# Kernel tuning notes

Hardware: AMD Instinct MI355X
Metric: run time of the kernel (lower is better)

The kernel has to match this reference:

```python
import jax, jax.numpy as jnp
import numpy as np

NUM_HEADS = 16
HEAD_SIZE = 64
N_EMBD = 1024


def setup_inputs() -> dict:
    key = jax.random.key(0)
    ks = jax.random.split(key, 7)
    B, T, S, C, H, D = 4, 1024, 1024, N_EMBD, NUM_HEADS, HEAD_SIZE
    s = 1.0 / np.sqrt(C)
    return {
        "x": jax.random.normal(ks[0], (B, T, C), jnp.float32),
        "y_enc": jax.random.normal(ks[1], (B, S, C), jnp.float32),
        # stacked per-head projection weights [H, C, D]
        "Wq": jax.random.normal(ks[2], (H, C, D), jnp.float32) * s,
        "Wk": jax.random.normal(ks[3], (H, C, D), jnp.float32) * s,
        "Wv": jax.random.normal(ks[4], (H, C, D), jnp.float32) * s,
        "Wo": jax.random.normal(ks[5], (C, C), jnp.float32) * s,
        "bo": jax.random.normal(ks[6], (C,), jnp.float32) * 0.01,
    }


def reference(x, y_enc, Wq, Wk, Wv, Wo, bo):
    B, T, C = x.shape
    # per-head projections (batched over heads)
    q = jnp.einsum("btc,hcd->bhtd", x, Wq)       # [B,H,T,D]
    k = jnp.einsum("bsc,hcd->bhsd", y_enc, Wk)   # [B,H,S,D]
    v = jnp.einsum("bsc,hcd->bhsd", y_enc, Wv)   # [B,H,S,D]
    # NOTE: original scales by C**-0.5 with C = n_embd (full embed dim)
    scale = C ** (-0.5)
    wei = jnp.einsum("bhtd,bhsd->bhts", q, k) * scale
    wei = jax.nn.softmax(wei, axis=-1)
    out = jnp.einsum("bhts,bhsd->bhtd", wei, v)  # [B,H,T,D]
    # concat heads along last dim == transpose + reshape
    out = out.transpose(0, 2, 1, 3).reshape(B, T, -1)  # [B,T,H*D]
    return out @ Wo.T + bo
```

## Files before the change

kernel.cpp:

```cpp
#include <hip/hip_runtime.h>
#include <hip/hip_bf16.h>

using u16 = unsigned short;
typedef short bf16x8 __attribute__((ext_vector_type(8)));
typedef float f32x4 __attribute__((ext_vector_type(4)));
typedef u16 u16x8 __attribute__((ext_vector_type(8)));
typedef u16 u16x4 __attribute__((ext_vector_type(4)));

#define B_ 4
#define T_ 1024
#define S_ 1024
#define C_ 1024
#define H_ 16
#define D_ 64
#define SCALE_LOG2E 0.0450842200f

#define AKSTR 40
#define KSTR  72

__device__ __forceinline__ u16 f2bf(float f) {
    __hip_bfloat16 h = __float2bfloat16(f);
    u16 u; __builtin_memcpy(&u, &h, 2); return u;
}
__device__ __forceinline__ float bf2f(u16 u) {
    __hip_bfloat16 h; __builtin_memcpy(&h, &u, 2);
    return __bfloat162float(h);
}
__device__ __forceinline__ u16x8 ldg8(const u16* p) { return *reinterpret_cast<const u16x8*>(p); }
__device__ __forceinline__ void sts8(u16* p, u16x8 v) { *reinterpret_cast<u16x8*>(p) = v; }
__device__ __forceinline__ bf16x8 lds8(const u16* p) { return *reinterpret_cast<const bf16x8*>(p); }

__global__ __launch_bounds__(256) void prep_kernel(const float* __restrict__ x,
                                                   const float* __restrict__ yenc,
                                                   const float* __restrict__ Wq,
                                                   const float* __restrict__ Wk,
                                                   const float* __restrict__ Wv,
                                                   const float* __restrict__ Wo,
                                                   u16* __restrict__ xbf,
                                                   u16* __restrict__ ybf,
                                                   u16* __restrict__ wtq,
                                                   u16* __restrict__ wtk,
                                                   u16* __restrict__ wtv,
                                                   u16* __restrict__ wohi,
                                                   u16* __restrict__ wolo) {
    const int z = blockIdx.z;
    const int t = threadIdx.x;
    if (z < 3) {
        __shared__ float ldsT[64][65];
        const float* W = (z == 0) ? Wq : (z == 1) ? Wk : Wv;
        u16* Wt = (z == 0) ? wtq : (z == 1) ? wtk : wtv;
        const int c0 = blockIdx.x * 64;
        const int h  = blockIdx.y;
        const float* Wh = W + (size_t)h * C_ * D_;
        u16* Wth = Wt + (size_t)h * D_ * C_;
        {
            int c = t >> 2;
            int d0 = (t & 3) * 16;
            #pragma unroll
            for (int q = 0; q < 4; ++q) {
                float4 v = *reinterpret_cast<const float4*>(Wh + (size_t)(c0 + c) * D_ + d0 + q * 4);
                ldsT[d0 + q * 4 + 0][c] = v.x;
                ldsT[d0 + q * 4 + 1][c] = v.y;
                ldsT[d0 + q * 4 + 2][c] = v.z;
                ldsT[d0 + q * 4 + 3][c] = v.w;
            }
        }
        __syncthreads();
        {
            int d = t >> 2;
            int cq = (t & 3) * 16;
            u16x8 o0, o1;
            #pragma unroll
            for (int j = 0; j < 8; ++j) o0[j] = f2bf(ldsT[d][cq + j]);
            #pragma unroll
            for (int j = 0; j < 8; ++j) o1[j] = f2bf(ldsT[d][cq + 8 + j]);
            *reinterpret_cast<u16x8*>(Wth + (size_t)d * C_ + c0 + cq) = o0;
            *reinterpret_cast<u16x8*>(Wth + (size_t)d * C_ + c0 + cq + 8) = o1;
        }
    } else if (z == 3) {
        int bid = blockIdx.y * 16 + blockIdx.x;
        #pragma unroll
        for (int it = 0; it < 4; ++it) {
            int i = (bid * 4 + it) * 256 + t;
            float4 v = reinterpret_cast<const float4*>(Wo)[i];
            float vv[4] = {v.x, v.y, v.z, v.w};
            u16x4 hh, ll;
            #pragma unroll
            for (int j = 0; j < 4; ++j) {
                u16 hb = f2bf(vv[j]);
                hh[j] = hb;
                ll[j] = f2bf(vv[j] - bf2f(hb));
            }
            reinterpret_cast<u16x4*>(wohi)[i] = hh;
            reinterpret_cast<u16x4*>(wolo)[i] = ll;
        }
    } else {
        const float* src = (z == 4) ? x : yenc;
        u16* dst = (z == 4) ? xbf : ybf;
        int bid = blockIdx.y * 16 + blockIdx.x;
        #pragma unroll
        for (int it = 0; it < 16; ++it) {
            int i = (bid * 16 + it) * 256 + t;
            float4 v = reinterpret_cast<const float4*>(src)[i];
            u16x4 o;
            o[0] = f2bf(v.x); o[1] = f2bf(v.y); o[2] = f2bf(v.z); o[3] = f2bf(v.w);
            reinterpret_cast<u16x4*>(dst)[i] = o;
        }
    }
}

__global__ __launch_bounds__(256) void proj_mfma_kernel(const u16* __restrict__ xbf,
                                                        const u16* __restrict__ ybf,
                                                        const u16* __restrict__ wtq,
                                                        const u16* __restrict__ wtk,
                                                        const u16* __restrict__ wtv,
                                                        u16* __restrict__ qb,
                                                        u16* __restrict__ kb,
                                                        u16* __restrict__ vtb) {
    __shared__ __align__(16) u16 Al[2][128 * AKSTR];
    __shared__ __align__(16) u16 Bl[2][128 * AKSTR];

    const int z = blockIdx.z;
    const u16* Xb = (z == 0) ? xbf : ybf;
    const u16* Wt = (z == 0) ? wtq : (z == 1) ? wtk : wtv;
    u16* out      = (z == 0) ? qb  : (z == 1) ? kb  : vtb;
    const bool transposed = (z == 2);

    const int n0  = blockIdx.x * 128;
    const int i0  = blockIdx.y * 128;
    const int tid = threadIdx.x;
    const int lane = tid & 63, w = tid >> 6;
    const int g = lane >> 4, li = lane & 15;
    const int wm = (w >> 1) * 64, wn = (w & 1) * 64;
    const int ar = tid >> 1, ac = (tid & 1) * 16;

    const u16* aSrc = Xb + (size_t)(i0 + ar) * C_ + ac;
    const u16* bSrc = Wt + (size_t)(n0 + ar) * C_ + ac;

    u16x8 ra0 = ldg8(aSrc), ra1 = ldg8(aSrc + 8);
    u16x8 rb0 = ldg8(bSrc), rb1 = ldg8(bSrc + 8);
    sts8(&Al[0][ar * AKSTR + ac], ra0);
    sts8(&Al[0][ar * AKSTR + ac + 8], ra1);
    sts8(&Bl[0][ar * AKSTR + ac], rb0);
    sts8(&Bl[0][ar * AKSTR + ac + 8], rb1);
    __syncthreads();

    f32x4 acc[4][4] = {};
    int cur = 0;
    for (int k0 = 0; k0 < C_; k0 += 32) {
        const bool has_next = (k0 + 32 < C_);
        if (has_next) {
            ra0 = ldg8(aSrc + k0 + 32);
            ra1 = ldg8(aSrc + k0 + 40);
            rb0 = ldg8(bSrc + k0 + 32);
            rb1 = ldg8(bSrc + k0 + 40);
        }

        bf16x8 a[4], b[4];
        #pragma unroll
        for (int mf = 0; mf < 4; ++mf)
            a[mf] = lds8(&Al[cur][(wm + mf * 16 + li) * AKSTR + g * 8]);
        #pragma unroll
        for (int nf = 0; nf < 4; ++nf)
            b[nf] = lds8(&Bl[cur][(wn + nf * 16 + li) * AKSTR + g * 8]);
        #pragma unroll
        for (int mf = 0; mf < 4; ++mf)
            #pragma unroll
            for (int nf = 0; nf < 4; ++nf)
                acc[mf][nf] = __builtin_amdgcn_mfma_f32_16x16x32_bf16(a[mf], b[nf], acc[mf][nf], 0, 0, 0);

        if (has_next) {
            sts8(&Al[cur ^ 1][ar * AKSTR + ac], ra0);
            sts8(&Al[cur ^ 1][ar * AKSTR + ac + 8], ra1);
            sts8(&Bl[cur ^ 1][ar * AKSTR + ac], rb0);
            sts8(&Bl[cur ^ 1][ar * AKSTR + ac + 8], rb1);
        }
        __syncthreads();
        cur ^= 1;
    }

    if (!transposed) {
        #pragma unroll
        for (int mf = 0; mf < 4; ++mf) {
            int gi = i0 + wm + mf * 16 + g * 4;
            #pragma unroll
            for (int r = 0; r < 4; ++r) {
                int m = gi + r;
                int b = m >> 10, tt = m & 1023;
                #pragma unroll
                for (int nf = 0; nf < 4; ++nf) {
                    int n = n0 + wn + nf * 16 + li;
                    int h = n >> 6, d = n & 63;
                    out[(((size_t)(b * H_ + h) * T_) + tt) * D_ + d] = f2bf(acc[mf][nf][r]);
                }
            }
        }
    } else {
        #pragma unroll
        for (int mf = 0; mf < 4; ++mf) {
            int gi = i0 + wm + mf * 16 + g * 4;
            int b = gi >> 10, s = gi & 1023;
            #pragma unroll
            for (int nf = 0; nf < 4; ++nf) {
                int n = n0 + wn + nf * 16 + li;
                int h = n >> 6, d = n & 63;
                u16x4 o;
                #pragma unroll
                for (int r = 0; r < 4; ++r) o[r] = f2bf(acc[mf][nf][r]);
                *reinterpret_cast<u16x4*>(out + (((size_t)(b * H_ + h) * D_) + d) * S_ + s) = o;
            }
        }
    }
}

__global__ __launch_bounds__(512) void attn_mfma_kernel(const u16* __restrict__ Q,
                                                        const u16* __restrict__ K,
                                                        const u16* __restrict__ Vt,
                                                        u16* __restrict__ out_hi,
                                                        u16* __restrict__ out_lo) {
    __shared__ __align__(16) u16 Kl[64 * KSTR];
    __shared__ __align__(16) u16 Vl[64 * KSTR];
    __shared__ __align__(16) u16 Pl[8][16 * KSTR];

    const int t0  = blockIdx.x * 128;
    const int h   = blockIdx.y;
    const int b   = blockIdx.z;
    const int tid = threadIdx.x;
    const int lane = tid & 63, w = tid >> 6;
    const int g = lane >> 4, li = lane & 15;

    const size_t bh = (size_t)(b * H_ + h);
    const u16* Qp = Q  + bh * T_ * D_;
    const u16* Kp = K  + bh * S_ * D_;
    const u16* Vp = Vt + bh * D_ * S_;

    bf16x8 qf[2];
    #pragma unroll
    for (int ks = 0; ks < 2; ++ks)
        qf[ks] = *reinterpret_cast<const bf16x8*>(
            Qp + (size_t)(t0 + w * 16 + li) * D_ + ks * 32 + g * 8);

    const int sr = tid >> 3, sc = (tid & 7) * 8;

    float lsum[4] = {};
    f32x4 accO[4] = {};

    for (int s0 = 0; s0 < S_; s0 += 64) {
        __syncthreads();
        *reinterpret_cast<u16x8*>(&Kl[sr * KSTR + sc]) =
            *reinterpret_cast<const u16x8*>(Kp + (size_t)(s0 + sr) * D_ + sc);
        *reinterpret_cast<u16x8*>(&Vl[sr * KSTR + sc]) =
            *reinterpret_cast<const u16x8*>(Vp + (size_t)sr * S_ + s0 + sc);
        __syncthreads();

        f32x4 scf[4] = {};
        #pragma unroll
        for (int nf = 0; nf < 4; ++nf)
            #pragma unroll
            for (int ks = 0; ks < 2; ++ks) {
                bf16x8 kf = *reinterpret_cast<const bf16x8*>(
                    &Kl[(nf * 16 + li) * KSTR + ks * 32 + g * 8]);
                scf[nf] = __builtin_amdgcn_mfma_f32_16x16x32_bf16(qf[ks], kf, scf[nf], 0, 0, 0);
            }

        u16* Pw = Pl[w];
        #pragma unroll
        for (int nf = 0; nf < 4; ++nf)
            #pragma unroll
            for (int r = 0; r < 4; ++r) {
                float p = exp2f(scf[nf][r] * SCALE_LOG2E);
                lsum[r] += p;
                Pw[(g * 4 + r) * KSTR + nf * 16 + li] = f2bf(p);
            }

        bf16x8 pf[2];
        #pragma unroll
        for (int ks = 0; ks < 2; ++ks)
            pf[ks] = *reinterpret_cast<const bf16x8*>(&Pl[w][li * KSTR + ks * 32 + g * 8]);

        #pragma unroll
        for (int nf = 0; nf < 4; ++nf)
            #pragma unroll
            for (int ks = 0; ks < 2; ++ks) {
                bf16x8 vf = *reinterpret_cast<const bf16x8*>(
                    &Vl[(nf * 16 + li) * KSTR + ks * 32 + g * 8]);
                accO[nf] = __builtin_amdgcn_mfma_f32_16x16x32_bf16(pf[ks], vf, accO[nf], 0, 0, 0);
            }
    }

    #pragma unroll
    for (int r = 0; r < 4; ++r) {
        #pragma unroll
        for (int off = 1; off < 16; off <<= 1)
            lsum[r] += __shfl_xor(lsum[r], off, 64);
    }

    #pragma unroll
    for (int r = 0; r < 4; ++r) {
        float inv = 1.0f / lsum[r];
        int tt = t0 + w * 16 + g * 4 + r;
        u16* dh = out_hi + ((size_t)(b * T_) + tt) * C_ + h * D_;
        u16* dl = out_lo + ((size_t)(b * T_) + tt) * C_ + h * D_;
        #pragma unroll
        for (int nf = 0; nf < 4; ++nf) {
            float v = accO[nf][r] * inv;
            u16 hb = f2bf(v);
            dh[nf * 16 + li] = hb;
            dl[nf * 16 + li] = f2bf(v - bf2f(hb));
        }
    }
}

__global__ __launch_bounds__(256) void outproj_mfma_kernel(const u16* __restrict__ Ahi,
                                                           const u16* __restrict__ Alo,
                                                           const u16* __restrict__ Bhi,
                                                           const u16* __restrict__ Blo,
                                                           const float* __restrict__ bo,
                                                           float* __restrict__ out) {
    __shared__ __align__(16) u16 AH[2][128 * AKSTR];
    __shared__ __align__(16) u16 AL[2][128 * AKSTR];
    __shared__ __align__(16) u16 BH[2][64 * AKSTR];
    __shared__ __align__(16) u16 BL[2][64 * AKSTR];

    const int n0  = blockIdx.x * 64;
    const int i0  = blockIdx.y * 128;
    const int tid = threadIdx.x;
    const int lane = tid & 63, w = tid >> 6;
    const int g = lane >> 4, li = lane & 15;
    const int wm = (w >> 1) * 64, wn = (w & 1) * 32;
    const int ar = tid >> 1, ac = (tid & 1) * 16;
    const int br = tid >> 2, bc = (tid & 3) * 8;

    const u16* ahSrc = Ahi + (size_t)(i0 + ar) * C_ + ac;
    const u16* alSrc = Alo + (size_t)(i0 + ar) * C_ + ac;
    const u16* bhSrc = Bhi + (size_t)(n0 + br) * C_ + bc;
    const u16* blSrc = Blo + (size_t)(n0 + br) * C_ + bc;

    u16x8 rh0 = ldg8(ahSrc), rh1 = ldg8(ahSrc + 8);
    u16x8 rl0 = ldg8(alSrc), rl1 = ldg8(alSrc + 8);
    u16x8 rbh = ldg8(bhSrc), rbl = ldg8(blSrc);
    sts8(&AH[0][ar * AKSTR + ac], rh0);
    sts8(&AH[0][ar * AKSTR + ac + 8], rh1);
    sts8(&AL[0][ar * AKSTR + ac], rl0);
    sts8(&AL[0][ar * AKSTR + ac + 8], rl1);
    sts8(&BH[0][br * AKSTR + bc], rbh);
    sts8(&BL[0][br * AKSTR + bc], rbl);
    __syncthreads();

    f32x4 acc[4][2] = {};
    int cur = 0;
    for (int k0 = 0; k0 < C_; k0 += 32) {
        const bool has_next = (k0 + 32 < C_);
        if (has_next) {
            rh0 = ldg8(ahSrc + k0 + 32);
            rh1 = ldg8(ahSrc + k0 + 40);
            rl0 = ldg8(alSrc + k0 + 32);
            rl1 = ldg8(alSrc + k0 + 40);
            rbh = ldg8(bhSrc + k0 + 32);
            rbl = ldg8(blSrc + k0 + 32);
        }

        bf16x8 ah[4], al[4], bh[2], bl[2];
        #pragma unroll
        for (int mf = 0; mf < 4; ++mf) {
            ah[mf] = lds8(&AH[cur][(wm + mf * 16 + li) * AKSTR + g * 8]);
            al[mf] = lds8(&AL[cur][(wm + mf * 16 + li) * AKSTR + g * 8]);
        }
        #pragma unroll
        for (int nf = 0; nf < 2; ++nf) {
            bh[nf] = lds8(&BH[cur][(wn + nf * 16 + li) * AKSTR + g * 8]);
            bl[nf] = lds8(&BL[cur][(wn + nf * 16 + li) * AKSTR + g * 8]);
        }
        #pragma unroll
        for (int mf = 0; mf < 4; ++mf)
            #pragma unroll
            for (int nf = 0; nf < 2; ++nf) {
                acc[mf][nf] = __builtin_amdgcn_mfma_f32_16x16x32_bf16(ah[mf], bh[nf], acc[mf][nf], 0, 0, 0);
                acc[mf][nf] = __builtin_amdgcn_mfma_f32_16x16x32_bf16(ah[mf], bl[nf], acc[mf][nf], 0, 0, 0);
                acc[mf][nf] = __builtin_amdgcn_mfma_f32_16x16x32_bf16(al[mf], bh[nf], acc[mf][nf], 0, 0, 0);
            }

        if (has_next) {
            sts8(&AH[cur ^ 1][ar * AKSTR + ac], rh0);
            sts8(&AH[cur ^ 1][ar * AKSTR + ac + 8], rh1);
            sts8(&AL[cur ^ 1][ar * AKSTR + ac], rl0);
            sts8(&AL[cur ^ 1][ar * AKSTR + ac + 8], rl1);
            sts8(&BH[cur ^ 1][br * AKSTR + bc], rbh);
            sts8(&BL[cur ^ 1][br * AKSTR + bc], rbl);
        }
        __syncthreads();
        cur ^= 1;
    }

    float bj[2];
    #pragma unroll
    for (int nf = 0; nf < 2; ++nf) bj[nf] = bo[n0 + wn + nf * 16 + li];
    #pragma unroll
    for (int mf = 0; mf < 4; ++mf) {
        int row = i0 + wm + mf * 16 + g * 4;
        #pragma unroll
        for (int r = 0; r < 4; ++r)
            #pragma unroll
            for (int nf = 0; nf < 2; ++nf)
                out[(size_t)(row + r) * C_ + n0 + wn + nf * 16 + li] = acc[mf][nf][r] + bj[nf];
    }
}

extern "C" void kernel_launch(void* const* d_in, const int* in_sizes, int n_in,
                              void* d_out, int out_size, void* d_ws, size_t ws_size,
                              hipStream_t stream) {
    const float* x    = (const float*)d_in[0];
    const float* yenc = (const float*)d_in[1];
    const float* Wq   = (const float*)d_in[2];
    const float* Wk   = (const float*)d_in[3];
    const float* Wv   = (const float*)d_in[4];
    const float* Wo   = (const float*)d_in[5];
    const float* bo   = (const float*)d_in[6];
    float* out = (float*)d_out;

    char* ws = (char*)d_ws;
    const size_t MB = 1024 * 1024;
    u16* xbf   = (u16*)(ws + 0 * MB);
    u16* ybf   = (u16*)(ws + 8 * MB);
    u16* wtq   = (u16*)(ws + 16 * MB);
    u16* wtk   = (u16*)(ws + 18 * MB);
    u16* wtv   = (u16*)(ws + 20 * MB);
    u16* wohi  = (u16*)(ws + 22 * MB);
    u16* wolo  = (u16*)(ws + 24 * MB);
    u16* qb    = (u16*)(ws + 26 * MB);
    u16* kb    = (u16*)(ws + 34 * MB);
    u16* vtb   = (u16*)(ws + 42 * MB);
    u16* ahi   = xbf;
    u16* alo   = ybf;

    prep_kernel<<<dim3(16, 16, 6), 256, 0, stream>>>(x, yenc, Wq, Wk, Wv, Wo,
                                                     xbf, ybf, wtq, wtk, wtv, wohi, wolo);

    proj_mfma_kernel<<<dim3(8, 32, 3), 256, 0, stream>>>(xbf, ybf, wtq, wtk, wtv, qb, kb, vtb);

    attn_mfma_kernel<<<dim3(T_ / 128, H_, B_), 512, 0, stream>>>(qb, kb, vtb, ahi, alo);

    outproj_mfma_kernel<<<dim3(16, 32), 256, 0, stream>>>(ahi, alo, wohi, wolo, bo, out);
}
```

Before: 214.3 us.

## Double-buffer K/V tiles in LDS with register prefetch in attention kernel

The attention kernel now keeps two LDS buffers for K and V. Each iteration loads the next tile from global memory into registers and writes it into the alternate buffer after the compute, so only one barrier per iteration is needed instead of two. The exp/P-store work is also split into two halves, each followed by its own PV MFMA chunk, so softmax and matrix work can interleave. The costs are double the K/V LDS footprint and extra live registers for the prefetch, which could lower occupancy.

```diff
diff --git a/kernel.cpp b/kernel.cpp
--- a/kernel.cpp
+++ b/kernel.cpp
@@ -218,8 +218,8 @@
                                                         const u16* __restrict__ Vt,
                                                         u16* __restrict__ out_hi,
                                                         u16* __restrict__ out_lo) {
-    __shared__ __align__(16) u16 Kl[64 * KSTR];
-    __shared__ __align__(16) u16 Vl[64 * KSTR];
+    __shared__ __align__(16) u16 Kl[2][64 * KSTR];
+    __shared__ __align__(16) u16 Vl[2][64 * KSTR];
     __shared__ __align__(16) u16 Pl[8][16 * KSTR];
 
     const int t0  = blockIdx.x * 128;
@@ -241,51 +241,75 @@
             Qp + (size_t)(t0 + w * 16 + li) * D_ + ks * 32 + g * 8);
 
     const int sr = tid >> 3, sc = (tid & 7) * 8;
+    const u16* kBase = Kp + (size_t)sr * D_ + sc;
+    const u16* vBase = Vp + (size_t)sr * S_ + sc;
+
+    u16x8 rk = ldg8(kBase);
+    u16x8 rv = ldg8(vBase);
+    sts8(&Kl[0][sr * KSTR + sc], rk);
+    sts8(&Vl[0][sr * KSTR + sc], rv);
+    __syncthreads();
 
     float lsum[4] = {};
     f32x4 accO[4] = {};
+    int cur = 0;
 
     for (int s0 = 0; s0 < S_; s0 += 64) {
-        __syncthreads();
-        *reinterpret_cast<u16x8*>(&Kl[sr * KSTR + sc]) =
-            *reinterpret_cast<const u16x8*>(Kp + (size_t)(s0 + sr) * D_ + sc);
-        *reinterpret_cast<u16x8*>(&Vl[sr * KSTR + sc]) =
-            *reinterpret_cast<const u16x8*>(Vp + (size_t)sr * S_ + s0 + sc);
-        __syncthreads();
+        const bool has_next = (s0 + 64 < S_);
+        if (has_next) {
+            rk = ldg8(kBase + (size_t)(s0 + 64) * D_);
+            rv = ldg8(vBase + s0 + 64);
+        }
 
         f32x4 scf[4] = {};
         #pragma unroll
         for (int nf = 0; nf < 4; ++nf)
             #pragma unroll
             for (int ks = 0; ks < 2; ++ks) {
-                bf16x8 kf = *reinterpret_cast<const bf16x8*>(
-                    &Kl[(nf * 16 + li) * KSTR + ks * 32 + g * 8]);
+                bf16x8 kf = lds8(&Kl[cur][(nf * 16 + li) * KSTR + ks * 32 + g * 8]);
                 scf[nf] = __builtin_amdgcn_mfma_f32_16x16x32_bf16(qf[ks], kf, scf[nf], 0, 0, 0);
             }
 
         u16* Pw = Pl[w];
         #pragma unroll
-        for (int nf = 0; nf < 4; ++nf)
+        for (int nf = 0; nf < 2; ++nf)
             #pragma unroll
             for (int r = 0; r < 4; ++r) {
                 float p = exp2f(scf[nf][r] * SCALE_LOG2E);
                 lsum[r] += p;
                 Pw[(g * 4 + r) * KSTR + nf * 16 + li] = f2bf(p);
             }
-
-        bf16x8 pf[2];
-        #pragma unroll
-        for (int ks = 0; ks < 2; ++ks)
-            pf[ks] = *reinterpret_cast<const bf16x8*>(&Pl[w][li * KSTR + ks * 32 + g * 8]);
-
-        #pragma unroll
-        for (int nf = 0; nf < 4; ++nf)
-            #pragma unroll
-            for (int ks = 0; ks < 2; ++ks) {
-                bf16x8 vf = *reinterpret_cast<const bf16x8*>(
-                    &Vl[(nf * 16 + li) * KSTR + ks * 32 + g * 8]);
-                accO[nf] = __builtin_amdgcn_mfma_f32_16x16x32_bf16(pf[ks], vf, accO[nf], 0, 0, 0);
-            }
+        {
+            bf16x8 pf0 = lds8(&Pl[w][li * KSTR + g * 8]);
+            #pragma unroll
+            for (int nf = 0; nf < 4; ++nf) {
+                bf16x8 vf = lds8(&Vl[cur][(nf * 16 + li) * KSTR + g * 8]);
+                accO[nf] = __builtin_amdgcn_mfma_f32_16x16x32_bf16(pf0, vf, accO[nf], 0, 0, 0);
+            }
+        }
+        #pragma unroll
+        for (int nf = 2; nf < 4; ++nf)
+            #pragma unroll
+            for (int r = 0; r < 4; ++r) {
+                float p = exp2f(scf[nf][r] * SCALE_LOG2E);
+                lsum[r] += p;
+                Pw[(g * 4 + r) * KSTR + nf * 16 + li] = f2bf(p);
+            }
+        {
+            bf16x8 pf1 = lds8(&Pl[w][li * KSTR + 32 + g * 8]);
+            #pragma unroll
+            for (int nf = 0; nf < 4; ++nf) {
+                bf16x8 vf = lds8(&Vl[cur][(nf * 16 + li) * KSTR + 32 + g * 8]);
+                accO[nf] = __builtin_amdgcn_mfma_f32_16x16x32_bf16(pf1, vf, accO[nf], 0, 0, 0);
+            }
+        }
+
+        if (has_next) {
+            sts8(&Kl[cur ^ 1][sr * KSTR + sc], rk);
+            sts8(&Vl[cur ^ 1][sr * KSTR + sc], rv);
+        }
+        __syncthreads();
+        cur ^= 1;
     }
 
     #pragma unroll
```

Result: no change. 212.5 us (-0.9%).
